# Kernel tuning notes

Measured on AMD Instinct MI355X. Metric: run time of the kernel, lower is better.

The kernel has to match this reference:

```python
import jax, jax.numpy as jnp
import numpy as np

DIM = -1
ALPHA = 1.5
N_ITERS = 100


def _p(z):
    # p(z) = clamp(z, min=0) ** (1 / (alpha - 1)); for alpha=1.5 this is square
    return jnp.maximum(z, 0.0) ** (1.0 / (ALPHA - 1.0))


def entmax_bisect(X):
    """Bisection search for the entmax threshold tau (entmax_bisect, alpha=1.5)."""
    am1 = ALPHA - 1.0
    d = X.shape[DIM]
    Xs = X * am1                                   # scaled logits
    max_val = jnp.max(Xs, axis=DIM, keepdims=True)
    tau_lo = max_val - 1.0                         # gp(1) = 1**(alpha-1) = 1
    tau_hi = max_val - (1.0 / d) ** am1            # gp(1/d)
    f_lo = jnp.sum(_p(Xs - tau_lo), axis=DIM, keepdims=True) - 1.0
    dm0 = tau_hi - tau_lo

    def body(i, carry):
        tau_lo, dm, _ = carry
        dm = dm * 0.5
        tau_m = tau_lo + dm
        p_m = _p(Xs - tau_m)
        f_m = jnp.sum(p_m, axis=DIM, keepdims=True) - 1.0
        tau_lo = jnp.where(f_m * f_lo >= 0.0, tau_m, tau_lo)
        return (tau_lo, dm, p_m)

    p0 = jnp.zeros_like(Xs)
    _, _, p_m = jax.lax.fori_loop(0, N_ITERS, body, (tau_lo, dm0, p0))
    # ensure_sum_one normalization (as in the entmax library forward)
    return p_m / jnp.sum(p_m, axis=DIM, keepdims=True)


def setup_inputs() -> dict:
    key = jax.random.key(0)
    x = jax.random.normal(key, (2, 1024, 32000), dtype=jnp.float32)
    return {"x": x}


def reference(x):
    # LogEntmaxBisect.forward: log(entmax_bisect(x, dim, alpha, iters))
    # zero-probability entries yield -inf, matching torch.log(0.)
    return jnp.log(entmax_bisect(x))
```

## Files before the change

### kernel.cpp

```cpp
#include <hip/hip_runtime.h>
#include <float.h>
#include <math.h>

#define D_DIM   32000
#define NT      256
#define CHUNKS  (D_DIM / 4)
#define KITER   ((CHUNKS + NT - 1) / NT)
#define NG4     (KITER / 4)
#define NWAVES  (NT / 64)
#define CAPW    1200

typedef float f32x4 __attribute__((ext_vector_type(4)));
typedef unsigned long long ull;

__device__ __forceinline__ float waveReduceSum(float v) {
#pragma unroll
    for (int m = 32; m >= 1; m >>= 1) v += __shfl_xor(v, m, 64);
    return v;
}

__device__ __forceinline__ float waveReduceMax(float v) {
#pragma unroll
    for (int m = 32; m >= 1; m >>= 1) v = fmaxf(v, __shfl_xor(v, m, 64));
    return v;
}

__device__ __forceinline__ float scrub_finite(float v) {
    const unsigned u = __float_as_uint(v);
    if ((u & 0x7f800000u) == 0x7f800000u) return -FLT_MAX;
    return v;
}

__device__ __forceinline__ float4 ldg4(const float4* __restrict__ p, int c) {
    if (c < CHUNKS) return p[c];
    float4 r; r.x = r.y = r.z = r.w = -FLT_MAX;
    return r;
}

__global__ __launch_bounds__(NT, 8)
void entmax_tau_kernel(const float* __restrict__ x, float* __restrict__ out, int rows)
{
    const int row = blockIdx.x;
    if (row >= rows) return;
    const size_t base = (size_t)row * D_DIM;
    const float4* __restrict__ xr4 = reinterpret_cast<const float4*>(x + base);

    __shared__ __align__(16) float s_pool[NWAVES * CAPW];
    __shared__ float s_red[NWAVES];
    __shared__ float s_S2[NWAVES];
    __shared__ float s_S1[NWAVES];
    __shared__ int   s_cnt[NWAVES];
    __shared__ int   s_flag;

    const int lane = threadIdx.x & 63;
    const int wv   = threadIdx.x >> 6;
    float* __restrict__ wpool = s_pool + wv * CAPW;
    const ull lmask = (1ull << lane) - 1ull;

    if (threadIdx.x == 0) s_flag = 0;
    __syncthreads();

    float runL  = -FLT_MAX;
    float waveM = -FLT_MAX;
    float pendR = -FLT_MAX;
    int n = 0;
    bool ovf = false;

    float4 cur[4], nxt[4];
#pragma unroll
    for (int j = 0; j < 4; ++j) cur[j] = ldg4(xr4, threadIdx.x + j * NT);

    for (int g = 0; g < NG4; ++g) {
        if (g + 1 < NG4) {
#pragma unroll
            for (int j = 0; j < 4; ++j)
                nxt[j] = ldg4(xr4, threadIdx.x + ((g + 1) * 4 + j) * NT);
        }
        float z[16];
#pragma unroll
        for (int j = 0; j < 4; ++j) {
            z[4 * j + 0] = cur[j].x; z[4 * j + 1] = cur[j].y;
            z[4 * j + 2] = cur[j].z; z[4 * j + 3] = cur[j].w;
        }
        float cm = z[0];
#pragma unroll
        for (int i = 1; i < 16; ++i) cm = fmaxf(cm, z[i]);
        runL = fmaxf(runL, cm);
        if ((g & 1) == 0) {
            waveM = fmaxf(waveM, pendR);
            pendR = waveReduceMax(runL);
        }

        float thrL = fmaxf(runL, waveM) - 2.0f;
        ull msk[16];
        int tot = 0;
#pragma unroll
        for (int j = 0; j < 16; ++j) {
            msk[j] = __ballot(z[j] > thrL);
            tot += __popcll(msk[j]);
        }
        if (tot) {
            if (n + tot > CAPW) {
                const float wfresh = waveReduceMax(runL);
                waveM = fmaxf(waveM, wfresh);
                const float thrW = wfresh - 2.0f;
                int nn = 0;
                for (int i = 0; i < n; i += 64) {
                    const float v = (i + lane < n) ? wpool[i + lane] : -FLT_MAX;
                    const ull km = __ballot(v > thrW);
                    const int r = __popcll(km & lmask);
                    if (v > thrW) wpool[nn + r] = v;
                    nn += __popcll(km);
                }
                n = nn;
                thrL = fmaxf(runL, waveM) - 2.0f;
                tot = 0;
#pragma unroll
                for (int j = 0; j < 16; ++j) {
                    msk[j] = __ballot(z[j] > thrL);
                    tot += __popcll(msk[j]);
                }
            }
            if (n + tot > CAPW) {
                ovf = true;
            } else {
#pragma unroll
                for (int j = 0; j < 16; ++j) {
                    if (z[j] > thrL) {
                        const int r = __popcll(msk[j] & lmask);
                        wpool[n + r] = z[j];
                    }
                    n += __popcll(msk[j]);
                }
            }
        }
#pragma unroll
        for (int j = 0; j < 4; ++j) cur[j] = nxt[j];
    }
    if (ovf && lane == 0) s_flag = 1;

    if (lane == 0) s_red[wv] = waveReduceMax(runL);
    __syncthreads();
    const float max_val = fmaxf(fmaxf(s_red[0], s_red[1]), fmaxf(s_red[2], s_red[3]));
    const int flag = s_flag;
    __syncthreads();

    const float u_lo0 = max_val - 2.0f;
    const float u_hi  = max_val - 0.011180339887498949f;

    if (!flag) {
        {
            int nn = 0;
            float a2 = 0.0f, a1 = 0.0f;
            for (int i = 0; i < n; i += 64) {
                const float v = (i + lane < n) ? wpool[i + lane] : -FLT_MAX;
                const ull km = __ballot(v > u_lo0);
                const int r = __popcll(km & lmask);
                if (v > u_lo0) wpool[nn + r] = v;
                nn += __popcll(km);
                const float t = fmaxf(v - u_lo0, 0.0f);
                a2 = fmaf(t, t, a2); a1 += t;
            }
            a2 = waveReduceSum(a2);
            a1 = waveReduceSum(a1);
            if (lane == 0) { s_cnt[wv] = nn; s_S2[wv] = a2; s_S1[wv] = a1; }
        }
        __syncthreads();
        if (wv != 0) return;

        const int n0 = s_cnt[0], n1 = s_cnt[1], n2 = s_cnt[2], n3 = s_cnt[3];
        float u  = u_lo0;
        float s_v = s_S2[0] + s_S2[1] + s_S2[2] + s_S2[3];
        float g  = s_v - 4.0f;
        float S1 = s_S1[0] + s_S1[1] + s_S1[2] + s_S1[3];

        for (int it = 0; it < 24 && g > 0.0f; ++it) {
            const float u_new = fminf(u + g / (2.0f * S1), u_hi);
            if (u_new == u) break;
            u = u_new;
            float S2 = 0.0f; S1 = 0.0f;
            {
                const float* __restrict__ pp0 = s_pool;
                for (int i = lane; i < n0; i += 64) {
                    const float t = fmaxf(pp0[i] - u, 0.0f);
                    S2 = fmaf(t, t, S2); S1 += t;
                }
                const float* __restrict__ pp1 = s_pool + CAPW;
                for (int i = lane; i < n1; i += 64) {
                    const float t = fmaxf(pp1[i] - u, 0.0f);
                    S2 = fmaf(t, t, S2); S1 += t;
                }
                const float* __restrict__ pp2 = s_pool + 2 * CAPW;
                for (int i = lane; i < n2; i += 64) {
                    const float t = fmaxf(pp2[i] - u, 0.0f);
                    S2 = fmaf(t, t, S2); S1 += t;
                }
                const float* __restrict__ pp3 = s_pool + 3 * CAPW;
                for (int i = lane; i < n3; i += 64) {
                    const float t = fmaxf(pp3[i] - u, 0.0f);
                    S2 = fmaf(t, t, S2); S1 += t;
                }
            }
            S2 = waveReduceSum(S2);
            S1 = waveReduceSum(S1);
            s_v = S2;
            g = S2 - 4.0f;
        }
        if (lane == 0) {
            float2 ts; ts.x = u; ts.y = s_v;
            *reinterpret_cast<float2*>(out + base) = ts;
        }
    } else {
        float u_lo = u_lo0;
        float acc = 0.0f;
        for (int k = 0; k < KITER; ++k) {
            const int c = threadIdx.x + k * NT;
            if (c < CHUNKS) {
                const float4 v = xr4[c];
                float t;
                t = fmaxf(v.x - u_lo, 0.0f); acc = fmaf(t, t, acc);
                t = fmaxf(v.y - u_lo, 0.0f); acc = fmaf(t, t, acc);
                t = fmaxf(v.z - u_lo, 0.0f); acc = fmaf(t, t, acc);
                t = fmaxf(v.w - u_lo, 0.0f); acc = fmaf(t, t, acc);
            }
        }
        acc = waveReduceSum(acc);
        if (lane == 0) s_red[wv] = acc;
        __syncthreads();
        const float f_lo = (s_red[0] + s_red[1] + s_red[2] + s_red[3]) - 4.0f;
        __syncthreads();

        float dm = u_hi - u_lo;
        float u_m = u_lo;
        float s_v = 4.0f;
        for (int it = 0; it < 100; ++it) {
            dm *= 0.5f;
            u_m = u_lo + dm;
            const bool fixed = (u_m == u_lo);
            float a = 0.0f;
            for (int k = 0; k < KITER; ++k) {
                const int c = threadIdx.x + k * NT;
                if (c < CHUNKS) {
                    const float4 v = xr4[c];
                    float t;
                    t = fmaxf(v.x - u_m, 0.0f); a = fmaf(t, t, a);
                    t = fmaxf(v.y - u_m, 0.0f); a = fmaf(t, t, a);
                    t = fmaxf(v.z - u_m, 0.0f); a = fmaf(t, t, a);
                    t = fmaxf(v.w - u_m, 0.0f); a = fmaf(t, t, a);
                }
            }
            a = waveReduceSum(a);
            if (lane == 0) s_red[wv] = a;
            __syncthreads();
            const float s = s_red[0] + s_red[1] + s_red[2] + s_red[3];
            __syncthreads();
            s_v = s;
            if ((s - 4.0f) * f_lo >= 0.0f) u_lo = u_m;
            if (fixed) break;
        }
        if (threadIdx.x == 0) {
            float2 ts; ts.x = u_m; ts.y = s_v;
            *reinterpret_cast<float2*>(out + base) = ts;
        }
    }
}

__global__ __launch_bounds__(NT, 8)
void entmax_finish_kernel(const float* __restrict__ x, float* __restrict__ out, int rows)
{
    const int row = blockIdx.x;
    if (row >= rows) return;
    const size_t base = (size_t)row * D_DIM;
    const f32x4* __restrict__ xv4 = reinterpret_cast<const f32x4*>(x + base);
    float* __restrict__ orow = out + base;

    __shared__ float2 s_ts;
    if (threadIdx.x == 0) s_ts = *reinterpret_cast<const float2*>(orow);
    __syncthreads();
    const float u_m = s_ts.x;
    const float inv_sv = 1.0f / s_ts.y;

    for (int k = 0; k < KITER; ++k) {
        const int c = threadIdx.x + k * NT;
        if (c < CHUNKS) {
            const f32x4 v = __builtin_nontemporal_load(xv4 + c);
            f32x4 o;
            {
                const float t = fmaxf(v.x - u_m, 0.0f);
                o.x = scrub_finite(__logf(fmaxf(t * t, 1e-35f) * inv_sv));
            }
            {
                const float t = fmaxf(v.y - u_m, 0.0f);
                o.y = scrub_finite(__logf(fmaxf(t * t, 1e-35f) * inv_sv));
            }
            {
                const float t = fmaxf(v.z - u_m, 0.0f);
                o.z = scrub_finite(__logf(fmaxf(t * t, 1e-35f) * inv_sv));
            }
            {
                const float t = fmaxf(v.w - u_m, 0.0f);
                o.w = scrub_finite(__logf(fmaxf(t * t, 1e-35f) * inv_sv));
            }
            __builtin_nontemporal_store(o, reinterpret_cast<f32x4*>(orow) + c);
        }
    }
}

extern "C" void kernel_launch(void* const* d_in, const int* in_sizes, int n_in,
                              void* d_out, int out_size, void* d_ws, size_t ws_size,
                              hipStream_t stream) {
    const float* x = (const float*)d_in[0];
    float* out = (float*)d_out;
    const int rows = in_sizes[0] / D_DIM;
    entmax_tau_kernel<<<dim3(rows), dim3(NT), 0, stream>>>(x, out, rows);
    entmax_finish_kernel<<<dim3(rows), dim3(NT), 0, stream>>>(x, out, rows);
}
```

Measured before the change: 159.1 us.

## Fuse tau search and log output into one kernel with two-pass candidate gather

Merges the threshold-search kernel and the finishing log kernel into a single launch that passes tau and the sum through shared memory instead of global memory. The single streaming pass with adaptive threshold pruning is replaced by a plain max pass followed by a second pass that gathers candidates above max-2 into shared memory while accumulating the Newton sums. The row is now read three times from global memory (likely L2-resident) instead of twice across kernels. The per-wave pool capacity shrinks, which can make the slow bisection fallback more likely if a wave holds many candidates.

```diff
diff --git a/kernel.cpp b/kernel.cpp
--- a/kernel.cpp
+++ b/kernel.cpp
@@ -6,9 +6,8 @@
 #define NT      256
 #define CHUNKS  (D_DIM / 4)
 #define KITER   ((CHUNKS + NT - 1) / NT)
-#define NG4     (KITER / 4)
 #define NWAVES  (NT / 64)
-#define CAPW    1200
+#define CAPW    1024
 
 typedef float f32x4 __attribute__((ext_vector_type(4)));
 typedef unsigned long long ull;
@@ -38,12 +37,13 @@
 }
 
 __global__ __launch_bounds__(NT, 8)
-void entmax_tau_kernel(const float* __restrict__ x, float* __restrict__ out, int rows)
+void entmax_log_fused(const float* __restrict__ x, float* __restrict__ out, int rows)
 {
     const int row = blockIdx.x;
     if (row >= rows) return;
     const size_t base = (size_t)row * D_DIM;
     const float4* __restrict__ xr4 = reinterpret_cast<const float4*>(x + base);
+    float* __restrict__ orow = out + base;
 
     __shared__ __align__(16) float s_pool[NWAVES * CAPW];
     __shared__ float s_red[NWAVES];
@@ -51,6 +51,7 @@
     __shared__ float s_S1[NWAVES];
     __shared__ int   s_cnt[NWAVES];
     __shared__ int   s_flag;
+    __shared__ float2 s_ts;
 
     const int lane = threadIdx.x & 63;
     const int wv   = threadIdx.x >> 6;
@@ -58,158 +59,99 @@
     const ull lmask = (1ull << lane) - 1ull;
 
     if (threadIdx.x == 0) s_flag = 0;
-    __syncthreads();
-
-    float runL  = -FLT_MAX;
-    float waveM = -FLT_MAX;
-    float pendR = -FLT_MAX;
-    int n = 0;
-    bool ovf = false;
-
-    float4 cur[4], nxt[4];
-#pragma unroll
-    for (int j = 0; j < 4; ++j) cur[j] = ldg4(xr4, threadIdx.x + j * NT);
-
-    for (int g = 0; g < NG4; ++g) {
-        if (g + 1 < NG4) {
-#pragma unroll
-            for (int j = 0; j < 4; ++j)
-                nxt[j] = ldg4(xr4, threadIdx.x + ((g + 1) * 4 + j) * NT);
-        }
-        float z[16];
-#pragma unroll
-        for (int j = 0; j < 4; ++j) {
-            z[4 * j + 0] = cur[j].x; z[4 * j + 1] = cur[j].y;
-            z[4 * j + 2] = cur[j].z; z[4 * j + 3] = cur[j].w;
-        }
-        float cm = z[0];
-#pragma unroll
-        for (int i = 1; i < 16; ++i) cm = fmaxf(cm, z[i]);
-        runL = fmaxf(runL, cm);
-        if ((g & 1) == 0) {
-            waveM = fmaxf(waveM, pendR);
-            pendR = waveReduceMax(runL);
-        }
-
-        float thrL = fmaxf(runL, waveM) - 2.0f;
-        ull msk[16];
-        int tot = 0;
-#pragma unroll
-        for (int j = 0; j < 16; ++j) {
-            msk[j] = __ballot(z[j] > thrL);
-            tot += __popcll(msk[j]);
-        }
-        if (tot) {
-            if (n + tot > CAPW) {
-                const float wfresh = waveReduceMax(runL);
-                waveM = fmaxf(waveM, wfresh);
-                const float thrW = wfresh - 2.0f;
-                int nn = 0;
-                for (int i = 0; i < n; i += 64) {
-                    const float v = (i + lane < n) ? wpool[i + lane] : -FLT_MAX;
-                    const ull km = __ballot(v > thrW);
-                    const int r = __popcll(km & lmask);
-                    if (v > thrW) wpool[nn + r] = v;
-                    nn += __popcll(km);
-                }
-                n = nn;
-                thrL = fmaxf(runL, waveM) - 2.0f;
-                tot = 0;
-#pragma unroll
-                for (int j = 0; j < 16; ++j) {
-                    msk[j] = __ballot(z[j] > thrL);
-                    tot += __popcll(msk[j]);
-                }
-            }
-            if (n + tot > CAPW) {
-                ovf = true;
-            } else {
-#pragma unroll
-                for (int j = 0; j < 16; ++j) {
-                    if (z[j] > thrL) {
-                        const int r = __popcll(msk[j] & lmask);
-                        wpool[n + r] = z[j];
-                    }
-                    n += __popcll(msk[j]);
-                }
-            }
-        }
-#pragma unroll
-        for (int j = 0; j < 4; ++j) cur[j] = nxt[j];
-    }
-    if (ovf && lane == 0) s_flag = 1;
-
-    if (lane == 0) s_red[wv] = waveReduceMax(runL);
+
+    float m0 = -FLT_MAX, m1 = -FLT_MAX, m2 = -FLT_MAX, m3 = -FLT_MAX;
+    for (int k = 0; k < KITER; ++k) {
+        const float4 v = ldg4(xr4, threadIdx.x + k * NT);
+        m0 = fmaxf(m0, v.x); m1 = fmaxf(m1, v.y);
+        m2 = fmaxf(m2, v.z); m3 = fmaxf(m3, v.w);
+    }
+    float m = fmaxf(fmaxf(m0, m1), fmaxf(m2, m3));
+    m = waveReduceMax(m);
+    if (lane == 0) s_red[wv] = m;
     __syncthreads();
     const float max_val = fmaxf(fmaxf(s_red[0], s_red[1]), fmaxf(s_red[2], s_red[3]));
-    const int flag = s_flag;
-    __syncthreads();
 
     const float u_lo0 = max_val - 2.0f;
     const float u_hi  = max_val - 0.011180339887498949f;
 
+    {
+        int n = 0;
+        float a2 = 0.0f, a1 = 0.0f;
+        for (int k = 0; k < KITER; ++k) {
+            const float4 v = ldg4(xr4, threadIdx.x + k * NT);
+#define ADMIT(zz)                                                          \
+            do {                                                           \
+                const float z_ = (zz);                                     \
+                const ull mk = __ballot(z_ > u_lo0);                       \
+                if (mk) {                                                  \
+                    if (z_ > u_lo0) {                                      \
+                        const int pos = n + __popcll(mk & lmask);          \
+                        if (pos < CAPW) wpool[pos] = z_;                   \
+                        const float t = z_ - u_lo0;                        \
+                        a2 = fmaf(t, t, a2); a1 += t;                      \
+                    }                                                      \
+                    n += __popcll(mk);                                     \
+                }                                                          \
+            } while (0)
+            ADMIT(v.x); ADMIT(v.y); ADMIT(v.z); ADMIT(v.w);
+#undef ADMIT
+        }
+        a2 = waveReduceSum(a2);
+        a1 = waveReduceSum(a1);
+        if (lane == 0) {
+            s_cnt[wv] = n;
+            s_S2[wv] = a2;
+            s_S1[wv] = a1;
+            if (n > CAPW) s_flag = 1;
+        }
+    }
+    __syncthreads();
+    const int flag = s_flag;
+
     if (!flag) {
-        {
-            int nn = 0;
-            float a2 = 0.0f, a1 = 0.0f;
-            for (int i = 0; i < n; i += 64) {
-                const float v = (i + lane < n) ? wpool[i + lane] : -FLT_MAX;
-                const ull km = __ballot(v > u_lo0);
-                const int r = __popcll(km & lmask);
-                if (v > u_lo0) wpool[nn + r] = v;
-                nn += __popcll(km);
-                const float t = fmaxf(v - u_lo0, 0.0f);
-                a2 = fmaf(t, t, a2); a1 += t;
-            }
-            a2 = waveReduceSum(a2);
-            a1 = waveReduceSum(a1);
-            if (lane == 0) { s_cnt[wv] = nn; s_S2[wv] = a2; s_S1[wv] = a1; }
-        }
-        __syncthreads();
-        if (wv != 0) return;
-
-        const int n0 = s_cnt[0], n1 = s_cnt[1], n2 = s_cnt[2], n3 = s_cnt[3];
-        float u  = u_lo0;
-        float s_v = s_S2[0] + s_S2[1] + s_S2[2] + s_S2[3];
-        float g  = s_v - 4.0f;
-        float S1 = s_S1[0] + s_S1[1] + s_S1[2] + s_S1[3];
-
-        for (int it = 0; it < 24 && g > 0.0f; ++it) {
-            const float u_new = fminf(u + g / (2.0f * S1), u_hi);
-            if (u_new == u) break;
-            u = u_new;
-            float S2 = 0.0f; S1 = 0.0f;
-            {
-                const float* __restrict__ pp0 = s_pool;
-                for (int i = lane; i < n0; i += 64) {
-                    const float t = fmaxf(pp0[i] - u, 0.0f);
-                    S2 = fmaf(t, t, S2); S1 += t;
+        if (wv == 0) {
+            const int n0 = s_cnt[0], n1 = s_cnt[1], n2 = s_cnt[2], n3 = s_cnt[3];
+            float u   = u_lo0;
+            float s_v = s_S2[0] + s_S2[1] + s_S2[2] + s_S2[3];
+            float g   = s_v - 4.0f;
+            float S1  = s_S1[0] + s_S1[1] + s_S1[2] + s_S1[3];
+
+            for (int it = 0; it < 24 && g > 0.0f; ++it) {
+                const float u_new = fminf(u + g / (2.0f * S1), u_hi);
+                if (u_new == u) break;
+                u = u_new;
+                float S2 = 0.0f; S1 = 0.0f;
+                {
+                    const float* __restrict__ pp0 = s_pool;
+                    for (int i = lane; i < n0; i += 64) {
+                        const float t = fmaxf(pp0[i] - u, 0.0f);
+                        S2 = fmaf(t, t, S2); S1 += t;
+                    }
+                    const float* __restrict__ pp1 = s_pool + CAPW;
+                    for (int i = lane; i < n1; i += 64) {
+                        const float t = fmaxf(pp1[i] - u, 0.0f);
+                        S2 = fmaf(t, t, S2); S1 += t;
+                    }
+                    const float* __restrict__ pp2 = s_pool + 2 * CAPW;
+                    for (int i = lane; i < n2; i += 64) {
+                        const float t = fmaxf(pp2[i] - u, 0.0f);
+                        S2 = fmaf(t, t, S2); S1 += t;
+                    }
+                    const float* __restrict__ pp3 = s_pool + 3 * CAPW;
+                    for (int i = lane; i < n3; i += 64) {
+                        const float t = fmaxf(pp3[i] - u, 0.0f);
+                        S2 = fmaf(t, t, S2); S1 += t;
+                    }
                 }
-                const float* __restrict__ pp1 = s_pool + CAPW;
-                for (int i = lane; i < n1; i += 64) {
-                    const float t = fmaxf(pp1[i] - u, 0.0f);
-                    S2 = fmaf(t, t, S2); S1 += t;
-                }
-                const float* __restrict__ pp2 = s_pool + 2 * CAPW;
-                for (int i = lane; i < n2; i += 64) {
-                    const float t = fmaxf(pp2[i] - u, 0.0f);
-                    S2 = fmaf(t, t, S2); S1 += t;
-                }
-                const float* __restrict__ pp3 = s_pool + 3 * CAPW;
-                for (int i = lane; i < n3; i += 64) {
-                    const float t = fmaxf(pp3[i] - u, 0.0f);
-                    S2 = fmaf(t, t, S2); S1 += t;
-                }
-            }
-            S2 = waveReduceSum(S2);
-            S1 = waveReduceSum(S1);
-            s_v = S2;
-            g = S2 - 4.0f;
-        }
-        if (lane == 0) {
-            float2 ts; ts.x = u; ts.y = s_v;
-            *reinterpret_cast<float2*>(out + base) = ts;
-        }
+                S2 = waveReduceSum(S2);
+                S1 = waveReduceSum(S1);
+                s_v = S2;
+                g = S2 - 4.0f;
+            }
+            if (lane == 0) { s_ts.x = u; s_ts.y = s_v; }
+        }
+        __syncthreads();
     } else {
         float u_lo = u_lo0;
         float acc = 0.0f;
@@ -258,28 +200,13 @@
             if ((s - 4.0f) * f_lo >= 0.0f) u_lo = u_m;
             if (fixed) break;
         }
-        if (threadIdx.x == 0) {
-            float2 ts; ts.x = u_m; ts.y = s_v;
-            *reinterpret_cast<float2*>(out + base) = ts;
-        }
-    }
-}
-
-__global__ __launch_bounds__(NT, 8)
-void entmax_finish_kernel(const float* __restrict__ x, float* __restrict__ out, int rows)
-{
-    const int row = blockIdx.x;
-    if (row >= rows) return;
-    const size_t base = (size_t)row * D_DIM;
-    const f32x4* __restrict__ xv4 = reinterpret_cast<const f32x4*>(x + base);
-    float* __restrict__ orow = out + base;
-
-    __shared__ float2 s_ts;
-    if (threadIdx.x == 0) s_ts = *reinterpret_cast<const float2*>(orow);
-    __syncthreads();
+        if (threadIdx.x == 0) { s_ts.x = u_m; s_ts.y = s_v; }
+        __syncthreads();
+    }
+
     const float u_m = s_ts.x;
     const float inv_sv = 1.0f / s_ts.y;
-
+    const f32x4* __restrict__ xv4 = reinterpret_cast<const f32x4*>(x + base);
     for (int k = 0; k < KITER; ++k) {
         const int c = threadIdx.x + k * NT;
         if (c < CHUNKS) {
@@ -312,6 +239,5 @@
     const float* x = (const float*)d_in[0];
     float* out = (float*)d_out;
     const int rows = in_sizes[0] / D_DIM;
-    entmax_tau_kernel<<<dim3(rows), dim3(NT), 0, stream>>>(x, out, rows);
-    entmax_finish_kernel<<<dim3(rows), dim3(NT), 0, stream>>>(x, out, rows);
-}
+    entmax_log_fused<<<dim3(rows), dim3(NT), 0, stream>>>(x, out, rows);
+}
```

New measurement: 240.7 us. +51.2%, slower.
